# Optimization experiments

Hardware: AMD Instinct MI355X
Metric: run time of the kernel (lower is better)

## Reference

```python
import jax, jax.numpy as jnp
import numpy as np

B, C, H, W = 16, 256, 32, 32
EPS = 1e-6


def setup_inputs() -> dict:
    key = jax.random.key(0)
    ks = jax.random.split(key, 6)
    s = 1.0 / np.sqrt(C)  # conv-like init scale
    return {
        "x": jax.random.normal(ks[0], (B, C, H, W), dtype=jnp.float32),
        "ln_w": jnp.ones((C,), dtype=jnp.float32),
        "ln_b": jnp.zeros((C,), dtype=jnp.float32),
        "wq": jax.random.normal(ks[1], (C, C), dtype=jnp.float32) * s,
        "bq": jnp.zeros((C,), dtype=jnp.float32),
        "wk": jax.random.normal(ks[2], (C, C), dtype=jnp.float32) * s,
        "bk": jnp.zeros((C,), dtype=jnp.float32),
        "wv": jax.random.normal(ks[3], (C, C), dtype=jnp.float32) * s,
        "bv": jnp.zeros((C,), dtype=jnp.float32),
        "wp": jax.random.normal(ks[4], (C, C), dtype=jnp.float32) * s,
        "bp": jnp.zeros((C,), dtype=jnp.float32),
    }


def reference(x, ln_w, ln_b, wq, bq, wk, bk, wv, bv, wp, bp):
    b, c, h, w = x.shape
    n = h * w
    # LayerNorm2d: normalize over channel dim (biased variance)
    mean = jnp.mean(x, axis=1, keepdims=True)
    var = jnp.var(x, axis=1, keepdims=True)
    hn = (x - mean) / jnp.sqrt(var + EPS)
    hn = hn * ln_w[None, :, None, None] + ln_b[None, :, None, None]
    hn = hn.reshape(b, c, n)  # [B, C, N]
    # 1x1 convs == channel matmuls; tokens layout [B, N, C]
    q = jnp.einsum('oc,bcn->bno', wq, hn) + bq  # [B, N, C]
    k = jnp.einsum('oc,bcn->bon', wk, hn) + bk[None, :, None]  # [B, C, N]
    v = jnp.einsum('oc,bcn->bno', wv, hn) + bv  # [B, N, C]
    scale = c ** (-0.5)
    attn = jnp.einsum('bnc,bcm->bnm', q, k) * scale  # [B, N, N]
    attn = jax.nn.softmax(attn, axis=-1)
    # dropout is identity in eval mode (deterministic reference)
    out = jnp.einsum('bnm,bmc->bnc', attn, v)  # [B, N, C]
    out = jnp.einsum('oc,bnc->bon', wp, out) + bp[None, :, None]  # [B, C, N]
    out = out.reshape(b, c, h, w)
    return x + out
```

## Files before the change

kernel.cpp:

```cpp
#include <hip/hip_runtime.h>
#include <hip/hip_bf16.h>
#include <stdint.h>
#include <math.h>

typedef __attribute__((ext_vector_type(8))) short bf8_t;
typedef __attribute__((ext_vector_type(4))) float f4_t;
typedef __attribute__((ext_vector_type(16))) float f16x_t;
typedef __attribute__((ext_vector_type(2))) unsigned u32x2;
typedef unsigned short u16;

#define GLOAD16(g, l) __builtin_amdgcn_global_load_lds(                                  \
    (const __attribute__((address_space(1))) void*)(g),                                  \
    (__attribute__((address_space(3))) void*)(l), 16, 0, 0)

#define KEEPALIVE(v) asm volatile("" : "+v"(v))

#define QSCALE 0.090168444f

__device__ __forceinline__ u16 f2bf(float f) {
    union { float f; unsigned u; } c; c.f = f;
    unsigned u = c.u;
    return (u16)((u + 0x7fffu + ((u >> 16) & 1u)) >> 16);
}

__device__ __forceinline__ unsigned cvt_pk_bf16(float lo, float hi_) {
    unsigned r;
    asm("v_cvt_pk_bf16_f32 %0, %1, %2" : "=v"(r) : "v"(lo), "v"(hi_));
    return r;
}

__device__ __forceinline__ void plswap(unsigned& a, unsigned& b) {
    u32x2 r = __builtin_amdgcn_permlane32_swap(a, b, false, false);
    a = r[0]; b = r[1];
}

__device__ __forceinline__ void pack_frags(const unsigned* pw, bf8_t& f0v, bf8_t& f1v) {
    unsigned w0 = pw[0], w1 = pw[1], w2 = pw[2], w3 = pw[3];
    unsigned u0 = pw[4], u1 = pw[5], u2 = pw[6], u3 = pw[7];
    plswap(w2, w0);
    plswap(w3, w1);
    plswap(u2, u0);
    plswap(u3, u1);
    union { unsigned w[4]; bf8_t v; } f0, f1;
    f0.w[0] = w0; f0.w[1] = w1; f0.w[2] = w2; f0.w[3] = w3;
    f1.w[0] = u0; f1.w[1] = u1; f1.w[2] = u2; f1.w[3] = u3;
    f0v = f0.v; f1v = f1.v;
}

__global__ void prep_kernel(const float* __restrict__ wq, const float* __restrict__ wk,
                            const float* __restrict__ wv, const float* __restrict__ wp,
                            const float* __restrict__ bq, const float* __restrict__ bk,
                            const float* __restrict__ bv,
                            u16* __restrict__ wcatT, u16* __restrict__ wpt,
                            float* __restrict__ biasc) {
    int idx = blockIdx.x * 256 + threadIdx.x;
    if (idx < 196608) {
        int o = idx >> 8, c = idx & 255;
        float v = (o < 256) ? wq[o * 256 + c]
                : (o < 512) ? wk[(o - 256) * 256 + c]
                            : wv[(o - 512) * 256 + c];
        wcatT[(((c >> 3) * 768) + o) * 8 + (c & 7)] = f2bf(v);
    } else if (idx < 262144) {
        int i = idx - 196608;
        int o = i >> 8, d = i & 255;
        wpt[(((d >> 3) * 256) + o) * 8 + (d & 7)] = f2bf(wp[i]);
    } else if (idx < 262912) {
        int i = idx - 262144;
        biasc[i] = (i < 256) ? bq[i] : (i < 512) ? bk[i - 256] : bv[i - 512];
    }
}

__global__ __launch_bounds__(256) void lnqkv_kernel(
    const float* __restrict__ x, const float* __restrict__ lw,
    const float* __restrict__ lb,
    const u16* __restrict__ wcatT, const float* __restrict__ biasc,
    u16* __restrict__ qbuf, u16* __restrict__ ktp, u16* __restrict__ vtp) {
    __shared__ u16 hn_lds[32 * 32 * 8];
    __shared__ float2 red[8][32];

    const int tid = threadIdx.x;
    const int bid = blockIdx.x;
    const int b = bid >> 5, n0 = (bid & 31) * 32;
    const int tok = tid & 31, cpart = tid >> 5;

    const float* xb = x + (size_t)b * 262144 + n0 + tok;
    float v[32];
    float s = 0.f, s2 = 0.f;
    #pragma unroll
    for (int i = 0; i < 32; i++) {
        v[i] = xb[(size_t)(cpart * 32 + i) * 1024];
        s += v[i]; s2 += v[i] * v[i];
    }
    red[cpart][tok] = make_float2(s, s2);
    __syncthreads();
    s = 0.f; s2 = 0.f;
    #pragma unroll
    for (int gi = 0; gi < 8; gi++) { float2 p = red[gi][tok]; s += p.x; s2 += p.y; }
    float mean = s * 0.00390625f;
    float rstd = rsqrtf(s2 * 0.00390625f - mean * mean + 1e-6f);
    #pragma unroll
    for (int j = 0; j < 4; j++) {
        bf8_t pk;
        #pragma unroll
        for (int e = 0; e < 8; e++) {
            int c = cpart * 32 + j * 8 + e;
            pk[e] = (short)f2bf((v[j * 8 + e] - mean) * rstd * lw[c] + lb[c]);
        }
        *(bf8_t*)&hn_lds[((cpart * 4 + j) * 32 + tok) * 8] = pk;
    }
    __syncthreads();

    const int lane = tid & 63, wv_ = tid >> 6;
    const int hi = lane >> 5, lq = lane & 31;
    const int n = n0 + lq;

    bf8_t hnf[16];
    #pragma unroll
    for (int tc = 0; tc < 16; tc++)
        hnf[tc] = *(const bf8_t*)&hn_lds[((tc * 2 + hi) * 32 + lq) * 8];
    #pragma unroll
    for (int tc = 0; tc < 16; tc++) KEEPALIVE(hnf[tc]);

    #pragma unroll
    for (int grp = 0; grp < 3; grp++) {
        #pragma unroll
        for (int sub = 0; sub < 2; sub++) {
            const int cb = grp * 256 + (wv_ * 2 + sub) * 32;
            bf8_t wf[16];
            #pragma unroll
            for (int tc = 0; tc < 16; tc++)
                wf[tc] = *(const bf8_t*)(wcatT + (((size_t)(tc * 2 + hi) * 768) + cb + lq) * 8);
            f16x_t acc = (f16x_t)0.0f;
            if (grp < 2) {
                #pragma unroll
                for (int tc = 0; tc < 16; tc++)
                    acc = __builtin_amdgcn_mfma_f32_32x32x16_bf16(wf[tc], hnf[tc], acc, 0, 0, 0);
                #pragma unroll
                for (int r = 0; r < 16; r++) {
                    float bv = biasc[cb + (r & 3) + 8 * (r >> 2) + 4 * hi];
                    acc[r] += bv;
                    if (grp == 0) acc[r] *= QSCALE;
                }
            } else {
                #pragma unroll
                for (int tc = 0; tc < 16; tc++)
                    acc = __builtin_amdgcn_mfma_f32_32x32x16_bf16(hnf[tc], wf[tc], acc, 0, 0, 0);
                float bv = biasc[cb + lq];
                #pragma unroll
                for (int r = 0; r < 16; r++) acc[r] += bv;
            }

            unsigned pw[8];
            #pragma unroll
            for (int j = 0; j < 8; j++) pw[j] = cvt_pk_bf16(acc[2 * j], acc[2 * j + 1]);
            bf8_t f0v, f1v;
            pack_frags(pw, f0v, f1v);

            if (grp == 0) {
                u16* qb = &qbuf[((size_t)b * 1024 + n) * 256 + cb];
                *(bf8_t*)(qb + hi * 8) = f0v;
                *(bf8_t*)(qb + 16 + hi * 8) = f1v;
            } else if (grp == 1) {
                int c0 = cb - 256 + hi * 8;
                *(bf8_t*)&ktp[(((size_t)b * 32 + (c0 >> 3)) * 1024 + n) * 8] = f0v;
                int c1 = c0 + 16;
                *(bf8_t*)&ktp[(((size_t)b * 32 + (c1 >> 3)) * 1024 + n) * 8] = f1v;
            } else {
                int d = cb - 512 + lq;
                int t0 = n0 + hi * 8;
                *(bf8_t*)&vtp[(((size_t)b * 128 + (t0 >> 3)) * 256 + d) * 8] = f0v;
                int t1 = t0 + 16;
                *(bf8_t*)&vtp[(((size_t)b * 128 + (t1 >> 3)) * 256 + d) * 8] = f1v;
            }
        }
    }
}

__global__ __launch_bounds__(512)
__attribute__((amdgpu_waves_per_eu(2, 2)))
void flash_kernel(const u16* __restrict__ qbuf,
                  const u16* __restrict__ kt,
                  const u16* __restrict__ vt3,
                  const u16* __restrict__ wpt,
                  const float* __restrict__ bp,
                  const float* __restrict__ x,
                  float* __restrict__ out) {
    __shared__ u16 K_lds[2][2][32 * 32 * 8];
    __shared__ u16 V_lds[2][2][4 * 256 * 8];
    __shared__ float lstat[2][32];

    const int flat = blockIdx.x;
    const int xcd = flat & 7, idx = flat >> 3;
    const int b = (xcd << 1) | (idx & 1);
    const int qb = idx >> 1;
    const int tid = threadIdx.x;
    const int wv = tid >> 6, lane = tid & 63;
    const int hi = lane >> 5, lq = lane & 31;
    const int qw = wv & 1, dw = (wv >> 1) & 1, g = wv >> 2;

    const int qrow = qb * 64 + qw * 32 + lq;
    const u16* qptr = qbuf + (size_t)(b * 1024 + qrow) * 256 + hi * 8;
    bf8_t qf[16];
    #pragma unroll
    for (int tc = 0; tc < 16; tc++) qf[tc] = *(const bf8_t*)(qptr + tc * 16);

    float l_r = 0.f;
    f16x_t o_acc[4];
    #pragma unroll
    for (int dt = 0; dt < 4; dt++) o_acc[dt] = (f16x_t)0.0f;

#define STAGE(T, BUF)                                                                     \
    {                                                                                     \
        _Pragma("unroll")                                                                 \
        for (int g2 = 0; g2 < 2; g2++) {                                                  \
            _Pragma("unroll")                                                             \
            for (int it = 0; it < 2; it++) {                                              \
                int cid = it * 512 + tid;                                                 \
                int chunk = cid >> 5, kvl = cid & 31;                                     \
                const u16* gk = kt + (((size_t)b * 32 + chunk) * 1024                     \
                                      + g2 * 512 + (T) * 32 + kvl) * 8;                   \
                GLOAD16(gk, &K_lds[g2][BUF][cid * 8]);                                    \
            }                                                                             \
            _Pragma("unroll")                                                             \
            for (int it = 0; it < 2; it++) {                                              \
                int cid = it * 512 + tid;                                                 \
                int kc = cid >> 8, d = cid & 255;                                         \
                const u16* gv = vt3 + (((size_t)b * 128 + g2 * 64 + (T) * 4 + kc) * 256   \
                                       + d) * 8;                                          \
                GLOAD16(gv, &V_lds[g2][BUF][cid * 8]);                                    \
            }                                                                             \
        }                                                                                 \
    }

    STAGE(0, 0);
    STAGE(1, 1);
    asm volatile("s_waitcnt vmcnt(8)" ::: "memory");
    __builtin_amdgcn_s_barrier();

    for (int t = 0; t < 16; ++t) {
        const int buf = t & 1;

        const u16* kb = &K_lds[g][buf][0];
        bf8_t kf[16];
        #pragma unroll
        for (int tc = 0; tc < 16; tc++)
            kf[tc] = *(const bf8_t*)(kb + ((tc * 2 + hi) * 32 + lq) * 8);
        #pragma unroll
        for (int tc = 0; tc < 16; tc++) KEEPALIVE(kf[tc]);

        f16x_t s0 = (f16x_t)0.0f, s1 = (f16x_t)0.0f;
        __builtin_amdgcn_s_setprio(1);
        #pragma unroll
        for (int tc = 0; tc < 8; tc++) {
            s0 = __builtin_amdgcn_mfma_f32_32x32x16_bf16(kf[2 * tc],     qf[2 * tc],     s0, 0, 0, 0);
            s1 = __builtin_amdgcn_mfma_f32_32x32x16_bf16(kf[2 * tc + 1], qf[2 * tc + 1], s1, 0, 0, 0);
        }
        __builtin_amdgcn_s_setprio(0);

        const u16* vb = &V_lds[g][buf][0];
        bf8_t vf[8];
        #pragma unroll
        for (int dt = 0; dt < 4; dt++) {
            int vrow = dw * 128 + dt * 32 + lq;
            vf[2 * dt]     = *(const bf8_t*)(vb + (hi * 256 + vrow) * 8);
            vf[2 * dt + 1] = *(const bf8_t*)(vb + ((2 + hi) * 256 + vrow) * 8);
        }
        #pragma unroll
        for (int j = 0; j < 8; j++) KEEPALIVE(vf[j]);

        f16x_t s = s0 + s1;

        float sum = 0.f;
        #pragma unroll
        for (int r = 0; r < 16; r++) { s[r] = exp2f(s[r]); sum += s[r]; }
        l_r += sum;

        unsigned pw[8];
        #pragma unroll
        for (int j = 0; j < 8; j++) pw[j] = cvt_pk_bf16(s[2 * j], s[2 * j + 1]);
        bf8_t f0v, f1v;
        pack_frags(pw, f0v, f1v);

        asm volatile("s_waitcnt vmcnt(0) lgkmcnt(0)" ::: "memory");
        __builtin_amdgcn_s_barrier();
        if (t < 14) STAGE(t + 2, buf);

        __builtin_amdgcn_s_setprio(1);
        #pragma unroll
        for (int dt = 0; dt < 4; dt++) {
            o_acc[dt] = __builtin_amdgcn_mfma_f32_32x32x16_bf16(vf[2 * dt],     f0v, o_acc[dt], 0, 0, 0);
            o_acc[dt] = __builtin_amdgcn_mfma_f32_32x32x16_bf16(vf[2 * dt + 1], f1v, o_acc[dt], 0, 0, 0);
        }
        __builtin_amdgcn_s_setprio(0);
    }

    __syncthreads();

    float l_tot = l_r + __shfl_xor(l_r, 32);
    float* obuf = (float*)&K_lds[0][0][0];
    float* rb = obuf + (qw * 2 + dw) * 4096;
    if (g == 1) {
        #pragma unroll
        for (int dt = 0; dt < 4; dt++)
            #pragma unroll
            for (int r = 0; r < 16; r++) {
                int drow = dt * 32 + (r & 3) + 8 * (r >> 2) + 4 * hi;
                rb[drow * 32 + lq] = o_acc[dt][r];
            }
        if (dw == 0 && hi == 0) lstat[qw][lq] = l_tot;
    }
    __syncthreads();

    bf8_t wpf[16];
    #pragma unroll
    for (int tc = 0; tc < 16; tc++)
        wpf[tc] = *(const bf8_t*)(wpt + (((tc * 2 + hi) * 256) + wv * 32 + lq) * 8);

    u16* O16 = (u16*)&V_lds[0][0][0];
    if (g == 0) {
        float inv = 1.0f / (l_tot + lstat[qw][lq]);
        #pragma unroll
        for (int dt = 0; dt < 4; dt++)
            #pragma unroll
            for (int r = 0; r < 16; r++) {
                int drow = dt * 32 + (r & 3) + 8 * (r >> 2) + 4 * hi;
                int d = dw * 128 + drow;
                float val = (o_acc[dt][r] + rb[drow * 32 + lq]) * inv;
                O16[((d >> 3) * 64 + qw * 32 + lq) * 8 + (d & 7)] = f2bf(val);
            }
    }
    __syncthreads();

    f16x_t p0 = (f16x_t)0.0f, p1 = (f16x_t)0.0f;
    __builtin_amdgcn_s_setprio(1);
    #pragma unroll
    for (int tc = 0; tc < 16; tc++) {
        bf8_t of0 = *(const bf8_t*)(O16 + ((tc * 2 + hi) * 64 + lq) * 8);
        bf8_t of1 = *(const bf8_t*)(O16 + ((tc * 2 + hi) * 64 + 32 + lq) * 8);
        p0 = __builtin_amdgcn_mfma_f32_32x32x16_bf16(wpf[tc], of0, p0, 0, 0, 0);
        p1 = __builtin_amdgcn_mfma_f32_32x32x16_bf16(wpf[tc], of1, p1, 0, 0, 0);
    }
    __builtin_amdgcn_s_setprio(0);
    #pragma unroll
    for (int r = 0; r < 16; r++) {
        int crow = wv * 32 + (r & 3) + 8 * (r >> 2) + 4 * hi;
        size_t base = ((size_t)b * 256 + crow) * 1024 + qb * 64;
        float bpv = bp[crow];
        out[base + lq]      = p0[r] + bpv + x[base + lq];
        out[base + 32 + lq] = p1[r] + bpv + x[base + 32 + lq];
    }
#undef STAGE
}

extern "C" void kernel_launch(void* const* d_in, const int* in_sizes, int n_in,
                              void* d_out, int out_size, void* d_ws, size_t ws_size,
                              hipStream_t stream) {
    (void)in_sizes; (void)n_in; (void)out_size; (void)ws_size;
    const float* x   = (const float*)d_in[0];
    const float* lnw = (const float*)d_in[1];
    const float* lnb = (const float*)d_in[2];
    const float* wq  = (const float*)d_in[3];
    const float* bq  = (const float*)d_in[4];
    const float* wk  = (const float*)d_in[5];
    const float* bk  = (const float*)d_in[6];
    const float* wv  = (const float*)d_in[7];
    const float* bv  = (const float*)d_in[8];
    const float* wp  = (const float*)d_in[9];
    const float* bp  = (const float*)d_in[10];
    float* out = (float*)d_out;

    char* ws = (char*)d_ws;
    u16*   wcatT = (u16*)(ws);
    u16*   wpt   = (u16*)(ws + 0x60000);
    float* biasc = (float*)(ws + 0x80000);
    u16*   qbuf  = (u16*)(ws + 0x90000);
    u16*   kt    = (u16*)(ws + 0x890000);
    u16*   vt3   = (u16*)(ws + 0x1090000);

    prep_kernel<<<1028, 256, 0, stream>>>(wq, wk, wv, wp, bq, bk, bv, wcatT, wpt, biasc);
    lnqkv_kernel<<<512, 256, 0, stream>>>(x, lnw, lnb, wcatT, biasc, qbuf, kt, vt3);
    flash_kernel<<<256, 512, 0, stream>>>(qbuf, kt, vt3, wpt, bp, x, out);
}
```

Measured before the change: 66.86 us.

## Halve flash block query tile, load V directly from global, drop V LDS staging

The flash kernel moves from 512-thread blocks covering 64 queries to 256-thread blocks covering 32 queries, doubling the grid to 512 blocks. V fragments are now read straight from global memory into registers each iteration, so the V LDS double buffer is gone. That frees LDS and aims for more resident blocks and better CU fill. The cost is that K tiles are reused by half as many queries, V global traffic per query roughly doubles, and global load latency now lands inside the loop.

New measurement: 103.3 us. 54.6% more time.

```diff
diff --git a/kernel.cpp b/kernel.cpp
--- a/kernel.cpp
+++ b/kernel.cpp
@@ -176,8 +176,7 @@
     }
 }
 
-__global__ __launch_bounds__(512)
-__attribute__((amdgpu_waves_per_eu(2, 2)))
+__global__ __launch_bounds__(256, 2)
 void flash_kernel(const u16* __restrict__ qbuf,
                   const u16* __restrict__ kt,
                   const u16* __restrict__ vt3,
@@ -186,19 +185,18 @@
                   const float* __restrict__ x,
                   float* __restrict__ out) {
     __shared__ u16 K_lds[2][2][32 * 32 * 8];
-    __shared__ u16 V_lds[2][2][4 * 256 * 8];
-    __shared__ float lstat[2][32];
+    __shared__ float lstat[32];
 
     const int flat = blockIdx.x;
     const int xcd = flat & 7, idx = flat >> 3;
     const int b = (xcd << 1) | (idx & 1);
-    const int qb = idx >> 1;
+    const int qt = idx >> 1;
     const int tid = threadIdx.x;
     const int wv = tid >> 6, lane = tid & 63;
     const int hi = lane >> 5, lq = lane & 31;
-    const int qw = wv & 1, dw = (wv >> 1) & 1, g = wv >> 2;
-
-    const int qrow = qb * 64 + qw * 32 + lq;
+    const int dw = wv & 1, g = wv >> 1;
+
+    const int qrow = qt * 32 + lq;
     const u16* qptr = qbuf + (size_t)(b * 1024 + qrow) * 256 + hi * 8;
     bf8_t qf[16];
     #pragma unroll
@@ -214,21 +212,13 @@
         _Pragma("unroll")                                                                 \
         for (int g2 = 0; g2 < 2; g2++) {                                                  \
             _Pragma("unroll")                                                             \
-            for (int it = 0; it < 2; it++) {                                              \
-                int cid = it * 512 + tid;                                                 \
+            for (int it = 0; it < 4; it++) {                                              \
+                int cid = it * 256 + tid;                                                 \
                 int chunk = cid >> 5, kvl = cid & 31;                                     \
                 const u16* gk = kt + (((size_t)b * 32 + chunk) * 1024                     \
                                       + g2 * 512 + (T) * 32 + kvl) * 8;                   \
                 GLOAD16(gk, &K_lds[g2][BUF][cid * 8]);                                    \
             }                                                                             \
-            _Pragma("unroll")                                                             \
-            for (int it = 0; it < 2; it++) {                                              \
-                int cid = it * 512 + tid;                                                 \
-                int kc = cid >> 8, d = cid & 255;                                         \
-                const u16* gv = vt3 + (((size_t)b * 128 + g2 * 64 + (T) * 4 + kc) * 256   \
-                                       + d) * 8;                                          \
-                GLOAD16(gv, &V_lds[g2][BUF][cid * 8]);                                    \
-            }                                                                             \
         }                                                                                 \
     }
 
@@ -248,6 +238,16 @@
         #pragma unroll
         for (int tc = 0; tc < 16; tc++) KEEPALIVE(kf[tc]);
 
+        bf8_t vf[8];
+        #pragma unroll
+        for (int dt = 0; dt < 4; dt++) {
+            int vrow = dw * 128 + dt * 32 + lq;
+            vf[2 * dt]     = *(const bf8_t*)(vt3 + (((size_t)b * 128 + g * 64 + t * 4 + hi) * 256 + vrow) * 8);
+            vf[2 * dt + 1] = *(const bf8_t*)(vt3 + (((size_t)b * 128 + g * 64 + t * 4 + 2 + hi) * 256 + vrow) * 8);
+        }
+        #pragma unroll
+        for (int j = 0; j < 8; j++) KEEPALIVE(vf[j]);
+
         f16x_t s0 = (f16x_t)0.0f, s1 = (f16x_t)0.0f;
         __builtin_amdgcn_s_setprio(1);
         #pragma unroll
@@ -257,17 +257,6 @@
         }
         __builtin_amdgcn_s_setprio(0);
 
-        const u16* vb = &V_lds[g][buf][0];
-        bf8_t vf[8];
-        #pragma unroll
-        for (int dt = 0; dt < 4; dt++) {
-            int vrow = dw * 128 + dt * 32 + lq;
-            vf[2 * dt]     = *(const bf8_t*)(vb + (hi * 256 + vrow) * 8);
-            vf[2 * dt + 1] = *(const bf8_t*)(vb + ((2 + hi) * 256 + vrow) * 8);
-        }
-        #pragma unroll
-        for (int j = 0; j < 8; j++) KEEPALIVE(vf[j]);
-
         f16x_t s = s0 + s1;
 
         float sum = 0.f;
@@ -298,7 +287,7 @@
 
     float l_tot = l_r + __shfl_xor(l_r, 32);
     float* obuf = (float*)&K_lds[0][0][0];
-    float* rb = obuf + (qw * 2 + dw) * 4096;
+    float* rb = obuf + dw * 4096;
     if (g == 1) {
         #pragma unroll
         for (int dt = 0; dt < 4; dt++)
@@ -307,18 +296,13 @@
                 int drow = dt * 32 + (r & 3) + 8 * (r >> 2) + 4 * hi;
                 rb[drow * 32 + lq] = o_acc[dt][r];
             }
-        if (dw == 0 && hi == 0) lstat[qw][lq] = l_tot;
-    }
-    __syncthreads();
-
-    bf8_t wpf[16];
-    #pragma unroll
-    for (int tc = 0; tc < 16; tc++)
-        wpf[tc] = *(const bf8_t*)(wpt + (((tc * 2 + hi) * 256) + wv * 32 + lq) * 8);
-
-    u16* O16 = (u16*)&V_lds[0][0][0];
+        if (dw == 0 && hi == 0) lstat[lq] = l_tot;
+    }
+    __syncthreads();
+
+    u16* O16 = (u16*)((char*)&K_lds[0][0][0] + 32768);
     if (g == 0) {
-        float inv = 1.0f / (l_tot + lstat[qw][lq]);
+        float inv = 1.0f / (l_tot + lstat[lq]);
         #pragma unroll
         for (int dt = 0; dt < 4; dt++)
             #pragma unroll
@@ -326,28 +310,32 @@
                 int drow = dt * 32 + (r & 3) + 8 * (r >> 2) + 4 * hi;
                 int d = dw * 128 + drow;
                 float val = (o_acc[dt][r] + rb[drow * 32 + lq]) * inv;
-                O16[((d >> 3) * 64 + qw * 32 + lq) * 8 + (d & 7)] = f2bf(val);
+                O16[((d >> 3) * 32 + lq) * 8 + (d & 7)] = f2bf(val);
             }
     }
     __syncthreads();
 
-    f16x_t p0 = (f16x_t)0.0f, p1 = (f16x_t)0.0f;
-    __builtin_amdgcn_s_setprio(1);
-    #pragma unroll
-    for (int tc = 0; tc < 16; tc++) {
-        bf8_t of0 = *(const bf8_t*)(O16 + ((tc * 2 + hi) * 64 + lq) * 8);
-        bf8_t of1 = *(const bf8_t*)(O16 + ((tc * 2 + hi) * 64 + 32 + lq) * 8);
-        p0 = __builtin_amdgcn_mfma_f32_32x32x16_bf16(wpf[tc], of0, p0, 0, 0, 0);
-        p1 = __builtin_amdgcn_mfma_f32_32x32x16_bf16(wpf[tc], of1, p1, 0, 0, 0);
-    }
-    __builtin_amdgcn_s_setprio(0);
-    #pragma unroll
-    for (int r = 0; r < 16; r++) {
-        int crow = wv * 32 + (r & 3) + 8 * (r >> 2) + 4 * hi;
-        size_t base = ((size_t)b * 256 + crow) * 1024 + qb * 64;
-        float bpv = bp[crow];
-        out[base + lq]      = p0[r] + bpv + x[base + lq];
-        out[base + 32 + lq] = p1[r] + bpv + x[base + 32 + lq];
+    #pragma unroll
+    for (int cset = 0; cset < 2; cset++) {
+        const int cb = wv * 64 + cset * 32;
+        bf8_t wpf[16];
+        #pragma unroll
+        for (int tc = 0; tc < 16; tc++)
+            wpf[tc] = *(const bf8_t*)(wpt + (((tc * 2 + hi) * 256) + cb + lq) * 8);
+        f16x_t p = (f16x_t)0.0f;
+        __builtin_amdgcn_s_setprio(1);
+        #pragma unroll
+        for (int tc = 0; tc < 16; tc++) {
+            bf8_t of = *(const bf8_t*)(O16 + ((tc * 2 + hi) * 32 + lq) * 8);
+            p = __builtin_amdgcn_mfma_f32_32x32x16_bf16(wpf[tc], of, p, 0, 0, 0);
+        }
+        __builtin_amdgcn_s_setprio(0);
+        #pragma unroll
+        for (int r = 0; r < 16; r++) {
+            int crow = cb + (r & 3) + 8 * (r >> 2) + 4 * hi;
+            size_t base = ((size_t)b * 256 + crow) * 1024 + qt * 32;
+            out[base + lq] = p[r] + bp[crow] + x[base + lq];
+        }
     }
 #undef STAGE
 }
@@ -379,5 +367,5 @@
 
     prep_kernel<<<1028, 256, 0, stream>>>(wq, wk, wv, wp, bq, bk, bv, wcatT, wpt, biasc);
     lnqkv_kernel<<<512, 256, 0, stream>>>(x, lnw, lnb, wcatT, biasc, qbuf, kt, vt3);
-    flash_kernel<<<256, 512, 0, stream>>>(qbuf, kt, vt3, wpt, bp, x, out);
-}
+    flash_kernel<<<512, 256, 0, stream>>>(qbuf, kt, vt3, wpt, bp, x, out);
+}
```
